# Optimization experiments

Hardware: AMD Instinct MI355X
Metric: run time of the kernel (lower is better)

The kernel has to match this reference:

```python
import jax, jax.numpy as jnp
import numpy as np

B, S, D, H = 4, 2048, 1024, 16
DH = D // H          # per-head attention size (attention_size // n_heads)
F = 4 * D            # FFN hidden
EPS = 1e-5


def _layer_norm(x, g, b):
    m = jnp.mean(x, axis=-1, keepdims=True)
    v = jnp.mean(jnp.square(x - m), axis=-1, keepdims=True)
    return (x - m) * jax.lax.rsqrt(v + EPS) * g + b


def setup_inputs() -> dict:
    key = jax.random.key(0)
    ks = jax.random.split(key, 12)
    s = 0.02
    x = jax.random.normal(ks[0], (B, S, D), dtype=jnp.float32)
    # causal mask: True = masked (strict upper triangle)
    mask = jnp.broadcast_to(jnp.triu(jnp.ones((S, S), dtype=bool), k=1), (B, S, S))
    wq = jax.random.normal(ks[1], (H, D, DH), dtype=jnp.float32) * s
    wk = jax.random.normal(ks[2], (H, D, DH), dtype=jnp.float32) * s
    wv = jax.random.normal(ks[3], (H, D, DH), dtype=jnp.float32) * s
    wo = jax.random.normal(ks[4], (D, D), dtype=jnp.float32) * s   # attention_size -> embedding_dim
    w1 = jax.random.normal(ks[5], (D, F), dtype=jnp.float32) * s
    b1 = jax.random.normal(ks[6], (F,), dtype=jnp.float32) * s
    w2 = jax.random.normal(ks[7], (F, D), dtype=jnp.float32) * s
    b2 = jax.random.normal(ks[8], (D,), dtype=jnp.float32) * s
    ln1_g = jnp.ones((D,), jnp.float32) + jax.random.normal(ks[9], (D,), jnp.float32) * s
    ln1_b = jax.random.normal(ks[10], (D,), jnp.float32) * s
    ln2_g = jnp.ones((D,), jnp.float32) + jax.random.normal(ks[11], (D,), jnp.float32) * s
    ln2_b = jnp.zeros((D,), jnp.float32)
    return {"x": x, "mask": mask, "wq": wq, "wk": wk, "wv": wv, "wo": wo,
            "w1": w1, "b1": b1, "w2": w2, "b2": b2,
            "ln1_g": ln1_g, "ln1_b": ln1_b, "ln2_g": ln2_g, "ln2_b": ln2_b}


def reference(x, mask, wq, wk, wv, wo, w1, b1, w2, b2, ln1_g, ln1_b, ln2_g, ln2_b):
    # --- self-attention block (pre-norm, residual) ---
    h = _layer_norm(x, ln1_g, ln1_b)                       # [B,S,D]
    q = jnp.einsum('bsd,hde->bhse', h, wq)                 # [B,H,S,DH]
    k = jnp.einsum('bsd,hde->bhse', h, wk)
    v = jnp.einsum('bsd,hde->bhse', h, wv)
    scores = jnp.einsum('bhse,bhte->bhst', q, k)           # [B,H,S,S]
    # faithful to source: mask-fill with -inf, THEN divide by sqrt(head_dim)
    scores = jnp.where(mask[:, None, :, :], -jnp.inf, scores) / jnp.sqrt(jnp.float32(DH))
    p = jax.nn.softmax(scores, axis=-1)
    attn = jnp.einsum('bhst,bhte->bhse', p, v)             # [B,H,S,DH]
    concat = attn.transpose(0, 2, 1, 3).reshape(B, S, D)   # heads concatenated on feature dim
    x = x + concat @ wo
    # --- feed-forward block ---
    h2 = _layer_norm(x, ln2_g, ln2_b)
    ff = jax.nn.gelu(h2 @ w1 + b1, approximate=False) @ w2 + b2
    return x + ff
```

## Files before the change

kernel.cpp:

```cpp
#include <hip/hip_runtime.h>
#include <hip/hip_bf16.h>
#include <math.h>


#define Bz 4
#define Sz 2048
#define Dz 1024
#define Hz 16
#define DHz 64
#define Fz 4096
#define Mz 8192

typedef float f32x4 __attribute__((ext_vector_type(4)));
typedef __bf16 bf16x8 __attribute__((ext_vector_type(8)));
typedef __bf16 bf16x4 __attribute__((ext_vector_type(4)));
typedef short s16x4 __attribute__((ext_vector_type(4)));

#define GLOAD_LDS16(g, l)                                                                   \
  __builtin_amdgcn_global_load_lds((const __attribute__((address_space(1))) unsigned int*)(g), \
                                   (__attribute__((address_space(3))) unsigned int*)(l), 16, 0, 0)

static __device__ __forceinline__ unsigned short f2bu(float f) {
  unsigned int u = __float_as_uint(f);
  u += 0x7fffu + ((u >> 16) & 1u);
  return (unsigned short)(u >> 16);
}

static __device__ __forceinline__ f32x4 mfma32(bf16x8 a, bf16x8 b, f32x4 c) {
  return __builtin_amdgcn_mfma_f32_16x16x32_bf16(a, b, c, 0, 0, 0);
}
static __device__ __forceinline__ f32x4 mfma16(s16x4 a, s16x4 b, f32x4 c) {
#if __has_builtin(__builtin_amdgcn_mfma_f32_16x16x16bf16_1k)
  return __builtin_amdgcn_mfma_f32_16x16x16bf16_1k(a, b, c, 0, 0, 0);
#else
  asm("v_mfma_f32_16x16x16_bf16 %0, %1, %2, %0" : "+v"(c) : "v"(a), "v"(b));
  return c;
#endif
}

template <int OFF>
static __device__ __forceinline__ s16x4 tr16(unsigned addr) {
  s16x4 r;
  asm volatile("ds_read_b64_tr_b16 %0, %1 offset:%2" : "=v"(r) : "v"(addr), "i"(OFF));
  return r;
}


__global__ __launch_bounds__(256) void pack_qkv(
    const float* __restrict__ wq, const float* __restrict__ wk, const float* __restrict__ wv,
    unsigned short* __restrict__ outW)
{
  __shared__ float tile[64][65];
  const int blk = blockIdx.x;
  const int dc = blk & 15;
  const int h  = (blk >> 4) & 15;
  const int p  = blk >> 8;
  const float* w = p == 0 ? wq : (p == 1 ? wk : wv);
  const int tid = threadIdx.x;
#pragma unroll
  for (int i = 0; i < 4; ++i) {
    int idx = i * 256 + tid;
    int dl = idx >> 4;
    int e0 = (idx & 15) * 4;
    const float4 v = *(const float4*)&w[(size_t)(h * 1024 + dc * 64 + dl) * 64 + e0];
    tile[dl][e0 + 0] = v.x; tile[dl][e0 + 1] = v.y;
    tile[dl][e0 + 2] = v.z; tile[dl][e0 + 3] = v.w;
  }
  __syncthreads();
#pragma unroll
  for (int i = 0; i < 4; ++i) {
    int idx = i * 256 + tid;
    int e = idx >> 4;
    int d0 = (idx & 15) * 4;
    ushort4 o;
    o.x = f2bu(tile[d0 + 0][e]); o.y = f2bu(tile[d0 + 1][e]);
    o.z = f2bu(tile[d0 + 2][e]); o.w = f2bu(tile[d0 + 3][e]);
    *(ushort4*)&outW[(size_t)(p * 1024 + h * 64 + e) * 1024 + dc * 64 + d0] = o;
  }
}

__global__ __launch_bounds__(256) void transpose_f32_to_bf16(
    const float* __restrict__ in, unsigned short* __restrict__ out, int R, int C)
{
  __shared__ float tile[32][33];
  int c0 = blockIdx.x * 32, r0 = blockIdx.y * 32;
  int x = threadIdx.x, y = threadIdx.y;
#pragma unroll
  for (int i = 0; i < 32; i += 8)
    tile[y + i][x] = in[(size_t)(r0 + y + i) * C + c0 + x];
  __syncthreads();
#pragma unroll
  for (int i = 0; i < 32; i += 8)
    out[(size_t)(c0 + y + i) * R + r0 + x] = f2bu(tile[x][y + i]);
}


__global__ __launch_bounds__(256) void ln_kernel(
    const float* __restrict__ x, const float* __restrict__ gamma, const float* __restrict__ beta,
    unsigned short* __restrict__ outH)
{
  const int row = blockIdx.x;
  const int tid = threadIdx.x;
  const float4 v = ((const float4*)(x + (size_t)row * Dz))[tid];
  float s = v.x + v.y + v.z + v.w;
  float s2 = v.x * v.x + v.y * v.y + v.z * v.z + v.w * v.w;
#pragma unroll
  for (int o = 32; o > 0; o >>= 1) {
    s += __shfl_xor(s, o);
    s2 += __shfl_xor(s2, o);
  }
  __shared__ float ss[4], ss2[4];
  if ((tid & 63) == 0) { ss[tid >> 6] = s; ss2[tid >> 6] = s2; }
  __syncthreads();
  s = ss[0] + ss[1] + ss[2] + ss[3];
  s2 = ss2[0] + ss2[1] + ss2[2] + ss2[3];
  const float mean = s * (1.0f / Dz);
  const float rstd = rsqrtf(s2 * (1.0f / Dz) - mean * mean + 1e-5f);
  const float4 g4 = ((const float4*)gamma)[tid];
  const float4 b4 = ((const float4*)beta)[tid];
  ushort4 o;
  o.x = f2bu((v.x - mean) * rstd * g4.x + b4.x);
  o.y = f2bu((v.y - mean) * rstd * g4.y + b4.y);
  o.z = f2bu((v.z - mean) * rstd * g4.z + b4.z);
  o.w = f2bu((v.w - mean) * rstd * g4.w + b4.w);
  ((ushort4*)(outH + (size_t)row * Dz))[tid] = o;
}


enum { EPI_BF16 = 0, EPI_GELU_BF16 = 1, EPI_RES_F32 = 2, EPI_BIAS_RES_F32 = 3 };

template <int BN, int EPI>
__global__ __launch_bounds__(512, 2) void gemm256(
    const unsigned short* __restrict__ A,
    const unsigned short* __restrict__ BT,
    int M, int N, int K,
    const float* bias, const float* resid,
    unsigned short* outb, float* outf)
{
  constexpr int BM = 256, BK = 64;
  constexpr int BCH = (BN * BK * 2) / (512 * 16);
  constexpr int NREP = BN / 64;
  __shared__ unsigned short As[2][BM * BK];
  __shared__ unsigned short Bs[2][BN * BK];

  const int tid = threadIdx.x;
  const int lane = tid & 63;
  const int wid = tid >> 6;
  const int wr = wid >> 2;
  const int wc = wid & 3;
  const int rsel = lane & 15;
  const int kgrp = lane >> 4;

  const int nwg = gridDim.x;
  const int bid = blockIdx.x;
  const int id2 = (bid & 7) * (nwg >> 3) + (bid >> 3);
  const int nbx = N / BN;
  const int n0 = (id2 % nbx) * BN;
  const int m0 = (id2 / nbx) * BM;

  f32x4 acc[8][NREP] = {};

  auto stA = [&](int kt, int b, int r) {
    int gc = r * 512 + tid;
    int row = gc >> 3;
    int kcs = (gc & 7) ^ (row & 7);
    GLOAD_LDS16(A + (size_t)(m0 + row) * K + kt * BK + kcs * 8, &As[b][gc * 8]);
  };
  auto stB = [&](int kt, int b, int r) {
    int gc = r * 512 + tid;
    int row = gc >> 3;
    int kcs = (gc & 7) ^ (row & 7);
    GLOAD_LDS16(BT + (size_t)(n0 + row) * K + kt * BK + kcs * 8, &Bs[b][gc * 8]);
  };

#pragma unroll
  for (int r = 0; r < BCH; ++r) stB(0, 0, r);
  stA(0, 0, 0); stA(0, 0, 2); stA(0, 0, 1); stA(0, 0, 3);
  asm volatile("s_waitcnt vmcnt(2)" ::: "memory");
  __builtin_amdgcn_sched_barrier(0);
  __builtin_amdgcn_s_barrier();

  const int T = K >> 6;
  for (int t = 0; t < T; ++t) {
    const int b = t & 1;
    const bool more = (t + 1 < T);
    const unsigned short* Ab = As[b];
    const unsigned short* Bb = Bs[b];
    bf16x8 bfr[NREP];
#pragma unroll
    for (int p = 0; p < 4; ++p) {
      const int kk = p >> 1, mh = p & 1;
      if (mh == 0) {
#pragma unroll
        for (int nf = 0; nf < NREP; ++nf) {
          int br = wc * (BN / 4) + nf * 16 + rsel;
          bfr[nf] = *(const bf16x8*)&Bb[br * BK + (((kk * 4 + kgrp) ^ (br & 7)) * 8)];
        }
      }
      bf16x8 af[4];
#pragma unroll
      for (int q = 0; q < 4; ++q) {
        int ar = wr * 128 + (mh * 4 + q) * 16 + rsel;
        af[q] = *(const bf16x8*)&Ab[ar * BK + (((kk * 4 + kgrp) ^ (ar & 7)) * 8)];
      }
      if (more) {
        if constexpr (BN == 256) {
          if (p == 0)      { stB(t + 1, b ^ 1, 0); stB(t + 1, b ^ 1, 1); }
          else if (p == 1) { stB(t + 1, b ^ 1, 2); stB(t + 1, b ^ 1, 3); }
          else if (p == 2) { stA(t + 1, b ^ 1, 0); stA(t + 1, b ^ 1, 2); }
          else             { stA(t + 1, b ^ 1, 1); stA(t + 1, b ^ 1, 3); }
        } else {
          if (p == 0)      { stB(t + 1, b ^ 1, 0); stB(t + 1, b ^ 1, 1); }
          else if (p == 1) { stA(t + 1, b ^ 1, 0); stA(t + 1, b ^ 1, 2); }
          else if (p == 2) { stA(t + 1, b ^ 1, 1); stA(t + 1, b ^ 1, 3); }
        }
      }
      if (p == 0 || p == 3) {
        if (more) asm volatile("s_waitcnt vmcnt(2)" ::: "memory");
        else      asm volatile("s_waitcnt vmcnt(0)" ::: "memory");
      }
      __builtin_amdgcn_sched_barrier(0);
      __builtin_amdgcn_s_barrier();
      asm volatile("s_waitcnt lgkmcnt(0)" ::: "memory");
      __builtin_amdgcn_sched_barrier(0);
      __builtin_amdgcn_s_setprio(1);
#pragma unroll
      for (int q = 0; q < 4; ++q)
#pragma unroll
        for (int nf = 0; nf < NREP; ++nf)
          acc[mh * 4 + q][nf] = mfma32(af[q], bfr[nf], acc[mh * 4 + q][nf]);
      __builtin_amdgcn_s_setprio(0);
      __builtin_amdgcn_sched_barrier(0);
      __builtin_amdgcn_s_barrier();
    }
  }

#pragma unroll
  for (int mf = 0; mf < 8; ++mf) {
#pragma unroll
    for (int nf = 0; nf < NREP; ++nf) {
      const int n = n0 + wc * (BN / 4) + nf * 16 + rsel;
#pragma unroll
      for (int j = 0; j < 4; ++j) {
        const int m = m0 + wr * 128 + mf * 16 + kgrp * 4 + j;
        const size_t idx = (size_t)m * N + n;
        float v = acc[mf][nf][j];
        if constexpr (EPI == EPI_BF16) {
          outb[idx] = f2bu(v);
        } else if constexpr (EPI == EPI_GELU_BF16) {
          v += bias[n];
          v = 0.5f * v * (1.0f + erff(v * 0.70710678118654752f));
          outb[idx] = f2bu(v);
        } else if constexpr (EPI == EPI_RES_F32) {
          outf[idx] = v + resid[idx];
        } else {
          outf[idx] = v + bias[n] + resid[idx];
        }
      }
    }
  }
}


__global__ __launch_bounds__(256, 2) void attn_kernel(
    const unsigned short* __restrict__ QKV,
    unsigned short* __restrict__ outA)
{
  __shared__ unsigned short Kt[64 * 64];
  __shared__ unsigned short Vs[64 * 64];
  const int ii = blockIdx.x;
  const int hh = blockIdx.y;
  const int bb = blockIdx.z;
  const int tid = threadIdx.x;
  const int lane = tid & 63;
  const int w = tid >> 6;
  const int rsel = lane & 15;
  const int kgrp = lane >> 4;
  const int qt[4] = {ii, 15 - ii, 16 + ii, 31 - ii};

  bf16x8 qf0[4], qf1[4];
  int qg[4];
#pragma unroll
  for (int s = 0; s < 4; ++s) {
    qg[s] = qt[s] * 64 + w * 16 + rsel;
    const size_t rowQ = (size_t)(bb * Sz + qg[s]) * 3072 + hh * 64;
    qf0[s] = *(const bf16x8*)&QKV[rowQ + kgrp * 8];
    qf1[s] = *(const bf16x8*)&QKV[rowQ + 32 + kgrp * 8];
  }

  f32x4 accO[4][4] = {};
  float mr[4] = {-INFINITY, -INFINITY, -INFINITY, -INFINITY};
  float lr[4] = {0.0f, 0.0f, 0.0f, 0.0f};

  auto vs3 = (__attribute__((address_space(3))) unsigned short*)Vs;
  const unsigned vbase = (unsigned)(uintptr_t)vs3 + (unsigned)lane * 8u;
  constexpr float SCL = 0.18033688011112042f;

  auto proc = [&](const bf16x8& q0, const bf16x8& q1, float& mrun, float& lrun,
                  f32x4* accS, s16x4* pb, bool edge, int qgs, int kb) {
    f32x4 sc[4];
    __builtin_amdgcn_s_setprio(1);
#pragma unroll
    for (int kf = 0; kf < 4; ++kf) {
      int key = kf * 16 + rsel;
      bf16x8 k0 = *(const bf16x8*)&Kt[key * 64 + ((kgrp ^ (key & 7)) * 8)];
      bf16x8 k1 = *(const bf16x8*)&Kt[key * 64 + (((4 + kgrp) ^ (key & 7)) * 8)];
      f32x4 s = {};
      s = mfma32(k0, q0, s);
      s = mfma32(k1, q1, s);
      sc[kf] = s;
    }
    __builtin_amdgcn_s_setprio(0);
    float tmax = -INFINITY;
#pragma unroll
    for (int kf = 0; kf < 4; ++kf)
#pragma unroll
      for (int j = 0; j < 4; ++j) {
        float v = sc[kf][j] * SCL;
        if (edge) {
          int keyg = kb + kf * 16 + kgrp * 4 + j;
          if (keyg > qgs) v = -INFINITY;
        }
        sc[kf][j] = v;
        tmax = fmaxf(tmax, v);
      }
    tmax = fmaxf(tmax, __shfl_xor(tmax, 16));
    tmax = fmaxf(tmax, __shfl_xor(tmax, 32));
    if (!__all(tmax <= mrun + 8.0f)) {
      const float mnew = fmaxf(mrun, tmax);
      const float corr = exp2f(mrun - mnew);
      lrun *= corr;
#pragma unroll
      for (int df = 0; df < 4; ++df) accS[df] *= corr;
      mrun = mnew;
    }
    float psum = 0.0f;
#pragma unroll
    for (int kf = 0; kf < 4; ++kf) {
      bf16x4 pv;
#pragma unroll
      for (int j = 0; j < 4; ++j) {
        float e = exp2f(sc[kf][j] - mrun);
        psum += e;
        pv[j] = (__bf16)e;
      }
      pb[kf] = __builtin_bit_cast(s16x4, pv);
    }
    psum += __shfl_xor(psum, 16);
    psum += __shfl_xor(psum, 32);
    lrun += psum;
  };

  for (int kt = 0; kt <= qt[3]; ++kt) {
    const int kb = kt * 64;
    if (kt) __syncthreads();
#pragma unroll
    for (int r = 0; r < 2; ++r) {
      int c = r * 256 + tid;
      int key = c >> 3;
      int dcs = (c & 7) ^ (key & 7);
      GLOAD_LDS16(QKV + (size_t)(bb * Sz + kb + key) * 3072 + 1024 + hh * 64 + dcs * 8,
                  &Kt[c * 8]);
    }
#pragma unroll
    for (int r = 0; r < 2; ++r) {
      int c = r * 256 + tid;
      int key = ((c >> 3) & 15) * 4 + ((c >> 1) & 3);
      int d = (c >> 7) * 16 + (c & 1) * 8;
      GLOAD_LDS16(QKV + (size_t)(bb * Sz + kb + key) * 3072 + 2048 + hh * 64 + d,
                  &Vs[c * 8]);
    }
    __syncthreads();

    s16x4 pb[4][4];
#pragma unroll
    for (int s = 0; s < 4; ++s)
      if (kt <= qt[s])
        proc(qf0[s], qf1[s], mr[s], lr[s], accO[s], pb[s], kt == qt[s], qg[s], kb);

#pragma unroll
    for (int df = 0; df < 4; ++df) {
      unsigned a = vbase + df * 2048;
      s16x4 vf0 = tr16<0>(a);
      s16x4 vf1 = tr16<512>(a);
      s16x4 vf2 = tr16<1024>(a);
      s16x4 vf3 = tr16<1536>(a);
      asm volatile("s_waitcnt lgkmcnt(0)" ::: "memory");
      __builtin_amdgcn_sched_barrier(0);
      __builtin_amdgcn_s_setprio(1);
#pragma unroll
      for (int s = 0; s < 4; ++s) {
        if (kt <= qt[s]) {
          accO[s][df] = mfma16(vf0, pb[s][0], accO[s][df]);
          accO[s][df] = mfma16(vf1, pb[s][1], accO[s][df]);
          accO[s][df] = mfma16(vf2, pb[s][2], accO[s][df]);
          accO[s][df] = mfma16(vf3, pb[s][3], accO[s][df]);
        }
      }
      __builtin_amdgcn_s_setprio(0);
    }
  }

#pragma unroll
  for (int s = 0; s < 4; ++s) {
    const float rl = 1.0f / lr[s];
    const size_t orow = (size_t)(bb * Sz + qg[s]) * Dz + hh * 64;
#pragma unroll
    for (int df = 0; df < 4; ++df) {
      s16x4 o;
#pragma unroll
      for (int j = 0; j < 4; ++j) o[j] = (short)f2bu(accO[s][df][j] * rl);
      *(s16x4*)&outA[orow + df * 16 + kgrp * 4] = o;
    }
  }
}


extern "C" void kernel_launch(void* const* d_in, const int* in_sizes, int n_in,
                              void* d_out, int out_size, void* d_ws, size_t ws_size,
                              hipStream_t stream) {
  const float* x   = (const float*)d_in[0];
  const float* wq  = (const float*)d_in[2];
  const float* wk  = (const float*)d_in[3];
  const float* wv  = (const float*)d_in[4];
  const float* wo  = (const float*)d_in[5];
  const float* w1  = (const float*)d_in[6];
  const float* b1  = (const float*)d_in[7];
  const float* w2  = (const float*)d_in[8];
  const float* b2  = (const float*)d_in[9];
  const float* g1  = (const float*)d_in[10];
  const float* be1 = (const float*)d_in[11];
  const float* g2  = (const float*)d_in[12];
  const float* be2 = (const float*)d_in[13];
  float* out = (float*)d_out;

  char* ws = (char*)d_ws;
  unsigned short* WqkvT = (unsigned short*)(ws);
  unsigned short* WoT   = (unsigned short*)(ws + 6291456);
  unsigned short* W1T   = (unsigned short*)(ws + 8388608);
  unsigned short* W2T   = (unsigned short*)(ws + 16777216);
  unsigned short* hbuf  = (unsigned short*)(ws + 25165824);
  unsigned short* big   = (unsigned short*)(ws + 41943040);

  dim3 tb(32, 8);
  pack_qkv<<<768, 256, 0, stream>>>(wq, wk, wv, WqkvT);
  transpose_f32_to_bf16<<<dim3(32, 32), tb, 0, stream>>>(wo, WoT, 1024, 1024);
  transpose_f32_to_bf16<<<dim3(128, 32), tb, 0, stream>>>(w1, W1T, 1024, 4096);
  transpose_f32_to_bf16<<<dim3(32, 128), tb, 0, stream>>>(w2, W2T, 4096, 1024);

  ln_kernel<<<Mz, 256, 0, stream>>>(x, g1, be1, hbuf);
  gemm256<128, EPI_BF16><<<768, 512, 0, stream>>>(
      hbuf, WqkvT, Mz, 3072, 1024, nullptr, nullptr, big, nullptr);
  attn_kernel<<<dim3(8, 16, 4), 256, 0, stream>>>(big, hbuf);
  gemm256<128, EPI_RES_F32><<<256, 512, 0, stream>>>(
      hbuf, WoT, Mz, 1024, 1024, nullptr, x, nullptr, out);
  ln_kernel<<<Mz, 256, 0, stream>>>(out, g2, be2, hbuf);
  gemm256<256, EPI_GELU_BF16><<<512, 512, 0, stream>>>(
      hbuf, W1T, Mz, Fz, 1024, b1, nullptr, big, nullptr);
  gemm256<128, EPI_BIAS_RES_F32><<<256, 512, 0, stream>>>(
      big, W2T, Mz, 1024, Fz, b2, out, nullptr, out);
}
```

Before: 459.9 us.

## Restructure GEMM to fixed BN=256 with variable BM and multi-stage prefetch pipeline

The GEMM kernel template now fixes BN at 256 and makes BM the parameter. For BM=128 it uses a three-deep LDS buffer ring, issuing loads DEPTH-1 tiles ahead with vmcnt-counted waits. The old per-phase interleaved stores and barriers are replaced by one wait and barrier per k-tile plus one trailing barrier. This aims to hide global-memory latency and cut barrier count, at the cost of more LDS for the deeper pipeline, which may limit occupancy. Call sites (not shown) must now pass BM instead of BN.

```diff
diff --git a/kernel.cpp b/kernel.cpp
--- a/kernel.cpp
+++ b/kernel.cpp
@@ -129,7 +129,7 @@
 
 enum { EPI_BF16 = 0, EPI_GELU_BF16 = 1, EPI_RES_F32 = 2, EPI_BIAS_RES_F32 = 3 };
 
-template <int BN, int EPI>
+template <int BM, int EPI>
 __global__ __launch_bounds__(512, 2) void gemm256(
     const unsigned short* __restrict__ A,
     const unsigned short* __restrict__ BT,
@@ -137,11 +137,15 @@
     const float* bias, const float* resid,
     unsigned short* outb, float* outf)
 {
-  constexpr int BM = 256, BK = 64;
+  constexpr int BN = 256, BK = 64;
+  constexpr int DEPTH = (BM == 128) ? 3 : 2;
+  constexpr int ACH = (BM * BK * 2) / (512 * 16);
   constexpr int BCH = (BN * BK * 2) / (512 * 16);
-  constexpr int NREP = BN / 64;
-  __shared__ unsigned short As[2][BM * BK];
-  __shared__ unsigned short Bs[2][BN * BK];
+  constexpr int NCH = ACH + BCH;
+  constexpr int MREP = BM / 32;
+  constexpr int NPH = (BM == 128) ? 2 : 4;
+  __shared__ unsigned short As[DEPTH][BM * BK];
+  __shared__ unsigned short Bs[DEPTH][BN * BK];
 
   const int tid = threadIdx.x;
   const int lane = tid & 63;
@@ -158,91 +162,88 @@
   const int n0 = (id2 % nbx) * BN;
   const int m0 = (id2 / nbx) * BM;
 
-  f32x4 acc[8][NREP] = {};
-
-  auto stA = [&](int kt, int b, int r) {
-    int gc = r * 512 + tid;
-    int row = gc >> 3;
-    int kcs = (gc & 7) ^ (row & 7);
-    GLOAD_LDS16(A + (size_t)(m0 + row) * K + kt * BK + kcs * 8, &As[b][gc * 8]);
+  f32x4 acc[MREP][4] = {};
+
+  auto issue = [&](int kt, int b) {
+#pragma unroll
+    for (int r = 0; r < ACH; ++r) {
+      int gc = r * 512 + tid;
+      int row = gc >> 3;
+      int kcs = (gc & 7) ^ (row & 7);
+      GLOAD_LDS16(A + (size_t)(m0 + row) * K + kt * BK + kcs * 8, &As[b][gc * 8]);
+    }
+#pragma unroll
+    for (int r = 0; r < BCH; ++r) {
+      int gc = r * 512 + tid;
+      int row = gc >> 3;
+      int kcs = (gc & 7) ^ (row & 7);
+      GLOAD_LDS16(BT + (size_t)(n0 + row) * K + kt * BK + kcs * 8, &Bs[b][gc * 8]);
+    }
   };
-  auto stB = [&](int kt, int b, int r) {
-    int gc = r * 512 + tid;
-    int row = gc >> 3;
-    int kcs = (gc & 7) ^ (row & 7);
-    GLOAD_LDS16(BT + (size_t)(n0 + row) * K + kt * BK + kcs * 8, &Bs[b][gc * 8]);
-  };
-
-#pragma unroll
-  for (int r = 0; r < BCH; ++r) stB(0, 0, r);
-  stA(0, 0, 0); stA(0, 0, 2); stA(0, 0, 1); stA(0, 0, 3);
-  asm volatile("s_waitcnt vmcnt(2)" ::: "memory");
-  __builtin_amdgcn_sched_barrier(0);
-  __builtin_amdgcn_s_barrier();
 
   const int T = K >> 6;
+#pragma unroll
+  for (int d = 0; d < DEPTH - 1; ++d) issue(d, d);
+
   for (int t = 0; t < T; ++t) {
-    const int b = t & 1;
-    const bool more = (t + 1 < T);
+    const int b = t % DEPTH;
+    if (t + DEPTH - 1 < T) issue(t + DEPTH - 1, (t + DEPTH - 1) % DEPTH);
+    int rem = T - 1 - t;
+    if (rem > DEPTH - 1) rem = DEPTH - 1;
+    if constexpr (DEPTH == 3) {
+      if (rem == 2)      asm volatile("s_waitcnt vmcnt(12)" ::: "memory");
+      else if (rem == 1) asm volatile("s_waitcnt vmcnt(6)" ::: "memory");
+      else               asm volatile("s_waitcnt vmcnt(0)" ::: "memory");
+    } else {
+      if (rem == 1) asm volatile("s_waitcnt vmcnt(8)" ::: "memory");
+      else          asm volatile("s_waitcnt vmcnt(0)" ::: "memory");
+    }
+    __builtin_amdgcn_sched_barrier(0);
+    __builtin_amdgcn_s_barrier();
+    __builtin_amdgcn_sched_barrier(0);
+
     const unsigned short* Ab = As[b];
     const unsigned short* Bb = Bs[b];
-    bf16x8 bfr[NREP];
-#pragma unroll
-    for (int p = 0; p < 4; ++p) {
-      const int kk = p >> 1, mh = p & 1;
+    bf16x8 bfr[4];
+#pragma unroll
+    for (int p = 0; p < NPH; ++p) {
+      const int kk = (NPH == 2) ? p : (p >> 1);
+      const int mh = (NPH == 2) ? 0 : (p & 1);
       if (mh == 0) {
 #pragma unroll
-        for (int nf = 0; nf < NREP; ++nf) {
-          int br = wc * (BN / 4) + nf * 16 + rsel;
+        for (int nf = 0; nf < 4; ++nf) {
+          int br = wc * 64 + nf * 16 + rsel;
           bfr[nf] = *(const bf16x8*)&Bb[br * BK + (((kk * 4 + kgrp) ^ (br & 7)) * 8)];
         }
       }
       bf16x8 af[4];
 #pragma unroll
       for (int q = 0; q < 4; ++q) {
-        int ar = wr * 128 + (mh * 4 + q) * 16 + rsel;
+        int ar = wr * (BM / 2) + (mh * 4 + q) * 16 + rsel;
         af[q] = *(const bf16x8*)&Ab[ar * BK + (((kk * 4 + kgrp) ^ (ar & 7)) * 8)];
       }
-      if (more) {
-        if constexpr (BN == 256) {
-          if (p == 0)      { stB(t + 1, b ^ 1, 0); stB(t + 1, b ^ 1, 1); }
-          else if (p == 1) { stB(t + 1, b ^ 1, 2); stB(t + 1, b ^ 1, 3); }
-          else if (p == 2) { stA(t + 1, b ^ 1, 0); stA(t + 1, b ^ 1, 2); }
-          else             { stA(t + 1, b ^ 1, 1); stA(t + 1, b ^ 1, 3); }
-        } else {
-          if (p == 0)      { stB(t + 1, b ^ 1, 0); stB(t + 1, b ^ 1, 1); }
-          else if (p == 1) { stA(t + 1, b ^ 1, 0); stA(t + 1, b ^ 1, 2); }
-          else if (p == 2) { stA(t + 1, b ^ 1, 1); stA(t + 1, b ^ 1, 3); }
-        }
-      }
-      if (p == 0 || p == 3) {
-        if (more) asm volatile("s_waitcnt vmcnt(2)" ::: "memory");
-        else      asm volatile("s_waitcnt vmcnt(0)" ::: "memory");
-      }
-      __builtin_amdgcn_sched_barrier(0);
-      __builtin_amdgcn_s_barrier();
       asm volatile("s_waitcnt lgkmcnt(0)" ::: "memory");
       __builtin_amdgcn_sched_barrier(0);
       __builtin_amdgcn_s_setprio(1);
 #pragma unroll
       for (int q = 0; q < 4; ++q)
 #pragma unroll
-        for (int nf = 0; nf < NREP; ++nf)
+        for (int nf = 0; nf < 4; ++nf)
           acc[mh * 4 + q][nf] = mfma32(af[q], bfr[nf], acc[mh * 4 + q][nf]);
       __builtin_amdgcn_s_setprio(0);
       __builtin_amdgcn_sched_barrier(0);
-      __builtin_amdgcn_s_barrier();
-    }
-  }
-
-#pragma unroll
-  for (int mf = 0; mf < 8; ++mf) {
-#pragma unroll
-    for (int nf = 0; nf < NREP; ++nf) {
-      const int n = n0 + wc * (BN / 4) + nf * 16 + rsel;
+    }
+    __builtin_amdgcn_s_barrier();
+  }
+
+#pragma unroll
+  for (int mf = 0; mf < MREP; ++mf) {
+#pragma unroll
+    for (int nf = 0; nf < 4; ++nf) {
+      const int n = n0 + wc * 64 + nf * 16 + rsel;
 #pragma unroll
       for (int j = 0; j < 4; ++j) {
-        const int m = m0 + wr * 128 + mf * 16 + kgrp * 4 + j;
+        const int m = m0 + wr * (BM / 2) + mf * 16 + kgrp * 4 + j;
         const size_t idx = (size_t)m * N + n;
         float v = acc[mf][nf][j];
         if constexpr (EPI == EPI_BF16) {
```

Result: no change. 460.4 us (+0.1%).
